# Kernel tuning notes

Hardware: AMD Instinct MI355X
Metric: run time of the kernel (lower is better)

The kernel has to match this reference:

```python
import jax, jax.numpy as jnp
import numpy as np

S, B, H = 2048, 16, 512      # seq_len, batch, hidden_size
L = 4096                     # total labels across batch
SMAX = 16                    # max span length
LAB = 256                    # label_size
V = 32000                    # len(voc)


def setup_inputs() -> dict:
    key = jax.random.key(0)
    ks = jax.random.split(key, 10)
    hidden = jax.random.normal(ks[0], (S, B, H), jnp.float32)
    begins = jax.random.randint(ks[1], (L,), 1, S - SMAX - 1)          # >=1 so begin-1 valid
    lens = jax.random.randint(ks[2], (L,), 1, SMAX + 1)                # span length in [1, SMAX]
    ends = begins + lens                                               # < S so hidden[end] valid
    bids = jax.random.randint(ks[3], (L,), 0, B)
    tags = jax.random.randint(ks[4], (L,), 0, V)
    sc = 0.02
    W1 = jax.random.normal(ks[5], (3 * H, LAB), jnp.float32) * sc
    b1 = jnp.zeros((LAB,), jnp.float32)
    W2 = jax.random.normal(ks[6], (LAB, LAB), jnp.float32) * sc
    b2 = jnp.zeros((LAB,), jnp.float32)
    Wo = jax.random.normal(ks[7], (LAB, V), jnp.float32) * sc
    bo = jnp.zeros((V,), jnp.float32)
    return dict(hidden=hidden, begins=begins, ends=ends, bids=bids, tags=tags,
                W1=W1, b1=b1, W2=W2, b2=b2, Wo=Wo, bo=bo)


def reference(hidden, begins, ends, bids, tags, W1, b1, W2, b2, Wo, bo):
    # --- batched span embed: gather + masked mean + boundary concat ---
    pos = begins[:, None] + jnp.arange(SMAX)            # [L, SMAX]
    valid = (pos < ends[:, None]).astype(hidden.dtype)  # [L, SMAX]
    posc = jnp.minimum(pos, S - 1)
    g = hidden[posc, bids[:, None]]                     # [L, SMAX, H] gather
    span_len = (ends - begins).astype(hidden.dtype)[:, None]
    mean = (g * valid[..., None]).sum(axis=1) / span_len           # [L, H]
    left = hidden[begins - 1, bids]                                 # [L, H]
    right = hidden[ends, bids]                                      # [L, H]
    span_emb = jnp.concatenate([left, mean, right], axis=-1)        # [L, 3H]
    # --- hidden2feature: Linear -> sigmoid -> Linear (dropout = eval identity) ---
    feat = jax.nn.sigmoid(span_emb @ W1 + b1) @ W2 + b2             # [L, LAB]
    # --- SoftmaxLoss: -log_softmax(h2o(feat)).gather(tags).mean() per label ---
    logp = jax.nn.log_softmax(feat @ Wo + bo, axis=-1)              # [L, V]
    per_label = -logp[jnp.arange(L), tags]                          # one tag per label
    return per_label.sum() / (L + 1e-5)
```

## Files before the change

### kernel.cpp

```cpp
#include <hip/hip_runtime.h>
#include <math.h>

#define S 2048
#define B 16
#define H 512
#define L 4096
#define SMAX 16
#define LAB 256
#define V 32000
#define NCH 250
#define LOG2E 1.44269504f

typedef __attribute__((ext_vector_type(8))) short short8;
typedef __attribute__((ext_vector_type(4))) float float4v;

__device__ inline ushort f2bf(float x) {
  union { float f; unsigned u; } c; c.f = x;
  unsigned r = c.u + 0x7fffu + ((c.u >> 16) & 1u);
  return (ushort)(r >> 16);
}
__device__ inline float bf2f(ushort h) {
  union { unsigned u; float f; } c; c.u = ((unsigned)h) << 16;
  return c.f;
}

__global__ __launch_bounds__(256) void spanb_kernel(
    const float* __restrict__ hidden, const int* __restrict__ begins,
    const int* __restrict__ ends, const int* __restrict__ bids,
    ushort* __restrict__ spanb) {
  int sub = threadIdx.x >> 7, t = threadIdx.x & 127;
  int l = blockIdx.x * 2 + sub;
  int b = bids[l], s0 = begins[l], s1 = ends[l];
  const float4* hidv = (const float4*)hidden;
  float4 lf = hidv[((size_t)(s0 - 1) * B + b) * 128 + t];
  float4 rf = hidv[((size_t)s1 * B + b) * 128 + t];
  float4 m = make_float4(0.f, 0.f, 0.f, 0.f);
  int len = s1 - s0;
  for (int j = 0; j < len; ++j) {
    float4 g = hidv[((size_t)(s0 + j) * B + b) * 128 + t];
    m.x += g.x; m.y += g.y; m.z += g.z; m.w += g.w;
  }
  float inv = 1.0f / (float)len;
  ushort* sp = spanb + (size_t)l * 1536;
  ushort4 u;
  u.x = f2bf(lf.x); u.y = f2bf(lf.y); u.z = f2bf(lf.z); u.w = f2bf(lf.w);
  *(ushort4*)&sp[t * 4] = u;
  u.x = f2bf(m.x * inv); u.y = f2bf(m.y * inv);
  u.z = f2bf(m.z * inv); u.w = f2bf(m.w * inv);
  *(ushort4*)&sp[512 + t * 4] = u;
  u.x = f2bf(rf.x); u.y = f2bf(rf.y); u.z = f2bf(rf.z); u.w = f2bf(rf.w);
  *(ushort4*)&sp[1024 + t * 4] = u;
}

__global__ __launch_bounds__(256) void tcast_kernel(
    const float* __restrict__ src, ushort* __restrict__ dst, int K, int N) {
  __shared__ ushort tile[64 * 72];
  int t = threadIdx.x;
  int n0 = blockIdx.x * 64;
  int k0 = blockIdx.y * 64;
  #pragma unroll
  for (int p = 0; p < 16; ++p) {
    int k = p * 4 + (t >> 6);
    int n = t & 63;
    tile[n * 72 + k] = f2bf(src[(size_t)(k0 + k) * N + n0 + n]);
  }
  __syncthreads();
  #pragma unroll
  for (int p = 0; p < 2; ++p) {
    int idx = p * 256 + t;
    int n = idx >> 3, c = idx & 7;
    *(uint4*)&dst[(size_t)(n0 + n) * K + k0 + c * 8] =
        *(const uint4*)&tile[n * 72 + c * 8];
  }
}

__global__ __launch_bounds__(256) void tcast_wo_kernel(
    const float* __restrict__ src, ushort* __restrict__ dst) {
  __shared__ ushort tile[64 * 72];
  int t = threadIdx.x;
  int n0 = blockIdx.x * 64;
  int k0 = blockIdx.y * 64;
  #pragma unroll
  for (int p = 0; p < 16; ++p) {
    int k = p * 4 + (t >> 6);
    int n = t & 63;
    tile[n * 72 + k] = f2bf(src[(size_t)(k0 + k) * V + n0 + n]);
  }
  __syncthreads();
  #pragma unroll
  for (int p = 0; p < 2; ++p) {
    int idx = p * 256 + t;
    int n = idx >> 3, c8 = idx & 7;
    int v = n0 + n, k = k0 + c8 * 8;
    int c = v >> 7, nt = (v >> 4) & 7, lr = v & 15;
    int kh = k >> 7, k4 = (k >> 5) & 3, lq = (k >> 3) & 3;
    size_t f = ((((size_t)c * 2 + kh) * 4 + k4) * 8 + nt) * 64 + lq * 16 + lr;
    *(uint4*)&dst[f * 8] = *(const uint4*)&tile[n * 72 + c8 * 8];
  }
}

__global__ __launch_bounds__(256) void feat_mfma_kernel(
    const ushort* __restrict__ spanb, const ushort* __restrict__ W1b,
    const float* __restrict__ b1, const ushort* __restrict__ W2b,
    const float* __restrict__ b2, ushort* __restrict__ featb) {
  __shared__ ushort Hs[16 * 264];
  int tid = threadIdx.x;
  int w = tid >> 6, lane = tid & 63;
  int lr = lane & 15, lq = lane >> 4;
  int l0 = blockIdx.x * 16;

  const short8* arow = (const short8*)(spanb + (size_t)(l0 + lr) * 1536 + lq * 8);
  const short8* brow[4];
  #pragma unroll
  for (int nt = 0; nt < 4; ++nt)
    brow[nt] = (const short8*)(W1b + (size_t)(w * 64 + nt * 16 + lr) * 1536 + lq * 8);

  float4v acc[4];
  float4v zero = {0.f, 0.f, 0.f, 0.f};
  #pragma unroll
  for (int nt = 0; nt < 4; ++nt) acc[nt] = zero;

  short8 af[2], bf[2][4];
  af[0] = arow[0];
  #pragma unroll
  for (int nt = 0; nt < 4; ++nt) bf[0][nt] = brow[nt][0];

  #pragma unroll
  for (int s = 0; s < 48; ++s) {
    int cur = s & 1, nxt = cur ^ 1;
    if (s < 47) {
      af[nxt] = arow[(s + 1) * 4];
      #pragma unroll
      for (int nt = 0; nt < 4; ++nt) bf[nxt][nt] = brow[nt][(s + 1) * 4];
    }
    #pragma unroll
    for (int nt = 0; nt < 4; ++nt)
      acc[nt] = __builtin_amdgcn_mfma_f32_16x16x32_bf16(
          af[cur], bf[cur][nt], acc[nt], 0, 0, 0);
  }

  {
    #pragma unroll
    for (int nt = 0; nt < 4; ++nt) {
      float b1v = b1[w * 64 + nt * 16 + lr];
      #pragma unroll
      for (int r = 0; r < 4; ++r) {
        int row = lq * 4 + r;
        float h = 1.0f / (1.0f + __expf(-(acc[nt][r] + b1v)));
        Hs[row * 264 + w * 64 + nt * 16 + lr] = f2bf(h);
      }
    }
  }
  __syncthreads();

  const short8* wrow[4];
  #pragma unroll
  for (int nt = 0; nt < 4; ++nt)
    wrow[nt] = (const short8*)(W2b + (size_t)(w * 64 + nt * 16 + lr) * 256 + lq * 8);

  float4v acc2[4];
  #pragma unroll
  for (int nt = 0; nt < 4; ++nt) acc2[nt] = zero;

  short8 bf2[2][4];
  #pragma unroll
  for (int nt = 0; nt < 4; ++nt) bf2[0][nt] = wrow[nt][0];

  #pragma unroll
  for (int s = 0; s < 8; ++s) {
    int cur = s & 1, nxt = cur ^ 1;
    if (s < 7) {
      #pragma unroll
      for (int nt = 0; nt < 4; ++nt) bf2[nxt][nt] = wrow[nt][(s + 1) * 4];
    }
    short8 af2 = *(const short8*)&Hs[lr * 264 + s * 32 + lq * 8];
    #pragma unroll
    for (int nt = 0; nt < 4; ++nt)
      acc2[nt] = __builtin_amdgcn_mfma_f32_16x16x32_bf16(
          af2, bf2[cur][nt], acc2[nt], 0, 0, 0);
  }

  {
    #pragma unroll
    for (int nt = 0; nt < 4; ++nt) {
      float b2v = b2[w * 64 + nt * 16 + lr];
      #pragma unroll
      for (int r = 0; r < 4; ++r) {
        int row = lq * 4 + r;
        int col = w * 64 + nt * 16 + lr;
        featb[(size_t)(l0 + row) * 256 + col] = f2bf(acc2[nt][r] + b2v);
      }
    }
  }
}

__global__ __launch_bounds__(256, 4) void logits2_kernel(
    const ushort* __restrict__ featb, const ushort* __restrict__ Wob,
    const float* __restrict__ bo, float* __restrict__ pz) {
  __shared__ ushort Blds[16384];
  int tid = threadIdx.x;
  int w = tid >> 6, lane = tid & 63;
  int lr = lane & 15, lq = lane >> 4;
  int l0 = blockIdx.x * 128;
  int v0 = blockIdx.y * 128;

  const short8* aptr[2];
  #pragma unroll
  for (int mt = 0; mt < 2; ++mt)
    aptr[mt] = (const short8*)(featb +
        (size_t)(l0 + w * 32 + mt * 16 + lr) * 256 + lq * 8);

  float4v acc[2][8];
  float4v zero = {0.f, 0.f, 0.f, 0.f};
  #pragma unroll
  for (int mt = 0; mt < 2; ++mt)
    #pragma unroll
    for (int nt = 0; nt < 8; ++nt) acc[mt][nt] = zero;

  short8 af[2][2];
  #pragma unroll
  for (int mt = 0; mt < 2; ++mt) af[0][mt] = aptr[mt][0];

  #pragma unroll
  for (int kh = 0; kh < 2; ++kh) {
    {
      const uint4* src4 = (const uint4*)(Wob +
          (size_t)blockIdx.y * 32768 + (size_t)kh * 16384);
      #pragma unroll
      for (int p = 0; p < 8; ++p) {
        int idx = p * 256 + tid;
        __builtin_amdgcn_global_load_lds(
            (const __attribute__((address_space(1))) unsigned int*)(src4 + idx),
            (__attribute__((address_space(3))) unsigned int*)&Blds[(size_t)idx * 8],
            16, 0, 0);
      }
    }
    __syncthreads();
    #pragma unroll
    for (int k4 = 0; k4 < 4; ++k4) {
      int kg = kh * 4 + k4;
      int cur = kg & 1, nxt = cur ^ 1;
      if (kg < 7) {
        #pragma unroll
        for (int mt = 0; mt < 2; ++mt)
          af[nxt][mt] = aptr[mt][(kg + 1) * 4];
      }
      short8 bf[8];
      #pragma unroll
      for (int nt = 0; nt < 8; ++nt)
        bf[nt] = *(const short8*)&Blds[(size_t)(((k4 * 8 + nt) * 64) + lane) * 8];
      __builtin_amdgcn_s_setprio(1);
      #pragma unroll
      for (int mt = 0; mt < 2; ++mt)
        #pragma unroll
        for (int nt = 0; nt < 8; ++nt)
          acc[mt][nt] = __builtin_amdgcn_mfma_f32_16x16x32_bf16(
              af[cur][mt], bf[nt], acc[mt][nt], 0, 0, 0);
      __builtin_amdgcn_s_setprio(0);
    }
    if (kh == 0) __syncthreads();
  }

  float bov[8];
  #pragma unroll
  for (int nt = 0; nt < 8; ++nt)
    bov[nt] = bo[v0 + nt * 16 + lr] * LOG2E;
  float z[2][4];
  #pragma unroll
  for (int mt = 0; mt < 2; ++mt)
    #pragma unroll
    for (int r = 0; r < 4; ++r) z[mt][r] = 0.f;
  #pragma unroll
  for (int mt = 0; mt < 2; ++mt)
    #pragma unroll
    for (int nt = 0; nt < 8; ++nt)
      #pragma unroll
      for (int r = 0; r < 4; ++r)
        z[mt][r] += exp2f(fmaf(acc[mt][nt][r], LOG2E, bov[nt]));
  #pragma unroll
  for (int mt = 0; mt < 2; ++mt)
    #pragma unroll
    for (int r = 0; r < 4; ++r) {
      #pragma unroll
      for (int off = 1; off < 16; off <<= 1)
        z[mt][r] += __shfl_xor(z[mt][r], off);
    }
  if (lr == 0) {
    int ch = blockIdx.y;
    #pragma unroll
    for (int mt = 0; mt < 2; ++mt) {
      float4 v4;
      v4.x = z[mt][0]; v4.y = z[mt][1]; v4.z = z[mt][2]; v4.w = z[mt][3];
      *(float4*)&pz[(size_t)ch * L + l0 + w * 32 + mt * 16 + lq * 4] = v4;
    }
  }
}

__global__ __launch_bounds__(256) void tag_kernel(
    const ushort* __restrict__ featb, const ushort* __restrict__ Wob,
    const float* __restrict__ bo, const int* __restrict__ tags,
    float* __restrict__ tagl) {
  int l = blockIdx.x * 4 + (threadIdx.x >> 6);
  int lane = threadIdx.x & 63;
  int tg = tags[l];
  int c = tg >> 7, nt = (tg >> 4) & 7, lr = tg & 15;
  int k0 = lane << 2;
  int kh = k0 >> 7, k4 = (k0 >> 5) & 3, lq = (k0 >> 3) & 3, e = k0 & 7;
  size_t f = ((((size_t)c * 2 + kh) * 4 + k4) * 8 + nt) * 64 + lq * 16 + lr;
  ushort4 wa = *(const ushort4*)&Wob[f * 8 + e];
  ushort4 fa = *(const ushort4*)&featb[(size_t)l * 256 + k0];
  float s = bf2f(fa.x) * bf2f(wa.x) + bf2f(fa.y) * bf2f(wa.y) +
            bf2f(fa.z) * bf2f(wa.z) + bf2f(fa.w) * bf2f(wa.w);
  #pragma unroll
  for (int off = 1; off < 64; off <<= 1) s += __shfl_xor(s, off);
  if (lane == 0) tagl[l] = s + bo[tg];
}

__global__ __launch_bounds__(256) void reduce_kernel(
    const float* __restrict__ pz, const float* __restrict__ tagl,
    float* __restrict__ out) {
  int l = blockIdx.x * 256 + threadIdx.x;
  float z = 0.f;
  for (int c = 0; c < NCH; ++c) z += pz[(size_t)c * L + l];
  float per = logf(z) - tagl[l];
  float v = per * (1.0f / (4096.0f + 1e-5f));
  #pragma unroll
  for (int off = 1; off < 64; off <<= 1) v += __shfl_xor(v, off);
  __shared__ float wsum[4];
  if ((threadIdx.x & 63) == 0) wsum[threadIdx.x >> 6] = v;
  __syncthreads();
  if (threadIdx.x == 0)
    atomicAdd(out, wsum[0] + wsum[1] + wsum[2] + wsum[3]);
}

extern "C" void kernel_launch(void* const* d_in, const int* in_sizes, int n_in,
                              void* d_out, int out_size, void* d_ws,
                              size_t ws_size, hipStream_t stream) {
  const float* hidden = (const float*)d_in[0];
  const int* begins = (const int*)d_in[1];
  const int* ends = (const int*)d_in[2];
  const int* bids = (const int*)d_in[3];
  const int* tags = (const int*)d_in[4];
  const float* W1 = (const float*)d_in[5];
  const float* b1 = (const float*)d_in[6];
  const float* W2 = (const float*)d_in[7];
  const float* b2 = (const float*)d_in[8];
  const float* Wo = (const float*)d_in[9];
  const float* bo = (const float*)d_in[10];
  float* out = (float*)d_out;

  ushort* featb = (ushort*)d_ws;
  ushort* Wob = featb + (size_t)L * 256;
  ushort* spanb = Wob + (size_t)V * 256;
  ushort* W1b = spanb + (size_t)L * 1536;
  ushort* W2b = W1b + (size_t)256 * 1536;
  float* pz = (float*)spanb;
  float* tagl = (float*)(W2b + (size_t)256 * 256);

  hipMemsetAsync(d_out, 0, sizeof(float), stream);
  spanb_kernel<<<L / 2, 256, 0, stream>>>(hidden, begins, ends, bids, spanb);
  tcast_kernel<<<dim3(4, 24), 256, 0, stream>>>(W1, W1b, 1536, LAB);
  tcast_kernel<<<dim3(4, 4), 256, 0, stream>>>(W2, W2b, LAB, LAB);
  tcast_wo_kernel<<<dim3(500, 4), 256, 0, stream>>>(Wo, Wob);
  feat_mfma_kernel<<<256, 256, 0, stream>>>(spanb, W1b, b1, W2b, b2, featb);
  logits2_kernel<<<dim3(32, NCH), 256, 0, stream>>>(featb, Wob, bo, pz);
  tag_kernel<<<L / 4, 256, 0, stream>>>(featb, Wob, bo, tags, tagl);
  reduce_kernel<<<L / 256, 256, 0, stream>>>(pz, tagl, out);
}
```

Before: 289.7 us.

## Merge prep kernels, fold tag dot into logits, process two vocab chunks per block

Span-embedding and the three weight cast/transposes are merged into one prep launch dispatched by block index. The memset is replaced by a write from the feature kernel, and the tag-logit kernel is folded into the logits launch as extra blocks. Each logits block now handles two 128-wide vocab chunks, prefetching the next chunk's first half while running the previous epilogue. This cuts launch count and hides some staging latency, at the cost of halving the logits grid and adding branch-divergent block roles.

```diff
diff --git a/kernel.cpp b/kernel.cpp
--- a/kernel.cpp
+++ b/kernel.cpp
@@ -24,40 +24,54 @@
   return c.f;
 }
 
-__global__ __launch_bounds__(256) void spanb_kernel(
+__global__ __launch_bounds__(256) void prep_kernel(
     const float* __restrict__ hidden, const int* __restrict__ begins,
     const int* __restrict__ ends, const int* __restrict__ bids,
-    ushort* __restrict__ spanb) {
-  int sub = threadIdx.x >> 7, t = threadIdx.x & 127;
-  int l = blockIdx.x * 2 + sub;
-  int b = bids[l], s0 = begins[l], s1 = ends[l];
-  const float4* hidv = (const float4*)hidden;
-  float4 lf = hidv[((size_t)(s0 - 1) * B + b) * 128 + t];
-  float4 rf = hidv[((size_t)s1 * B + b) * 128 + t];
-  float4 m = make_float4(0.f, 0.f, 0.f, 0.f);
-  int len = s1 - s0;
-  for (int j = 0; j < len; ++j) {
-    float4 g = hidv[((size_t)(s0 + j) * B + b) * 128 + t];
-    m.x += g.x; m.y += g.y; m.z += g.z; m.w += g.w;
-  }
-  float inv = 1.0f / (float)len;
-  ushort* sp = spanb + (size_t)l * 1536;
-  ushort4 u;
-  u.x = f2bf(lf.x); u.y = f2bf(lf.y); u.z = f2bf(lf.z); u.w = f2bf(lf.w);
-  *(ushort4*)&sp[t * 4] = u;
-  u.x = f2bf(m.x * inv); u.y = f2bf(m.y * inv);
-  u.z = f2bf(m.z * inv); u.w = f2bf(m.w * inv);
-  *(ushort4*)&sp[512 + t * 4] = u;
-  u.x = f2bf(rf.x); u.y = f2bf(rf.y); u.z = f2bf(rf.z); u.w = f2bf(rf.w);
-  *(ushort4*)&sp[1024 + t * 4] = u;
-}
-
-__global__ __launch_bounds__(256) void tcast_kernel(
-    const float* __restrict__ src, ushort* __restrict__ dst, int K, int N) {
+    ushort* __restrict__ spanb, const float* __restrict__ W1,
+    ushort* __restrict__ W1b, const float* __restrict__ W2,
+    ushort* __restrict__ W2b, const float* __restrict__ Wo,
+    ushort* __restrict__ Wob) {
   __shared__ ushort tile[64 * 72];
+  int bid = blockIdx.x;
   int t = threadIdx.x;
-  int n0 = blockIdx.x * 64;
-  int k0 = blockIdx.y * 64;
+
+  if (bid < 2048) {
+    int sub = t >> 7, tt = t & 127;
+    int l = bid * 2 + sub;
+    int b = bids[l], s0 = begins[l], s1 = ends[l];
+    const float4* hidv = (const float4*)hidden;
+    float4 lf = hidv[((size_t)(s0 - 1) * B + b) * 128 + tt];
+    float4 rf = hidv[((size_t)s1 * B + b) * 128 + tt];
+    float4 m = make_float4(0.f, 0.f, 0.f, 0.f);
+    int len = s1 - s0;
+    for (int j = 0; j < len; ++j) {
+      float4 g = hidv[((size_t)(s0 + j) * B + b) * 128 + tt];
+      m.x += g.x; m.y += g.y; m.z += g.z; m.w += g.w;
+    }
+    float inv = 1.0f / (float)len;
+    ushort* sp = spanb + (size_t)l * 1536;
+    ushort4 u;
+    u.x = f2bf(lf.x); u.y = f2bf(lf.y); u.z = f2bf(lf.z); u.w = f2bf(lf.w);
+    *(ushort4*)&sp[tt * 4] = u;
+    u.x = f2bf(m.x * inv); u.y = f2bf(m.y * inv);
+    u.z = f2bf(m.z * inv); u.w = f2bf(m.w * inv);
+    *(ushort4*)&sp[512 + tt * 4] = u;
+    u.x = f2bf(rf.x); u.y = f2bf(rf.y); u.z = f2bf(rf.z); u.w = f2bf(rf.w);
+    *(ushort4*)&sp[1024 + tt * 4] = u;
+    return;
+  }
+
+  const float* src; ushort* dst; int K, N, n0, k0; bool wo = false;
+  if (bid < 2144) {
+    int u = bid - 2048; src = W1; dst = W1b; K = 1536; N = 256;
+    n0 = (u & 3) * 64; k0 = (u >> 2) * 64;
+  } else if (bid < 2160) {
+    int u = bid - 2144; src = W2; dst = W2b; K = 256; N = 256;
+    n0 = (u & 3) * 64; k0 = (u >> 2) * 64;
+  } else {
+    int u = bid - 2160; src = Wo; dst = Wob; K = 256; N = V;
+    n0 = (u % 500) * 64; k0 = (u / 500) * 64; wo = true;
+  }
   #pragma unroll
   for (int p = 0; p < 16; ++p) {
     int k = p * 4 + (t >> 6);
@@ -65,46 +79,36 @@
     tile[n * 72 + k] = f2bf(src[(size_t)(k0 + k) * N + n0 + n]);
   }
   __syncthreads();
-  #pragma unroll
-  for (int p = 0; p < 2; ++p) {
-    int idx = p * 256 + t;
-    int n = idx >> 3, c = idx & 7;
-    *(uint4*)&dst[(size_t)(n0 + n) * K + k0 + c * 8] =
-        *(const uint4*)&tile[n * 72 + c * 8];
-  }
-}
-
-__global__ __launch_bounds__(256) void tcast_wo_kernel(
-    const float* __restrict__ src, ushort* __restrict__ dst) {
-  __shared__ ushort tile[64 * 72];
-  int t = threadIdx.x;
-  int n0 = blockIdx.x * 64;
-  int k0 = blockIdx.y * 64;
-  #pragma unroll
-  for (int p = 0; p < 16; ++p) {
-    int k = p * 4 + (t >> 6);
-    int n = t & 63;
-    tile[n * 72 + k] = f2bf(src[(size_t)(k0 + k) * V + n0 + n]);
-  }
-  __syncthreads();
-  #pragma unroll
-  for (int p = 0; p < 2; ++p) {
-    int idx = p * 256 + t;
-    int n = idx >> 3, c8 = idx & 7;
-    int v = n0 + n, k = k0 + c8 * 8;
-    int c = v >> 7, nt = (v >> 4) & 7, lr = v & 15;
-    int kh = k >> 7, k4 = (k >> 5) & 3, lq = (k >> 3) & 3;
-    size_t f = ((((size_t)c * 2 + kh) * 4 + k4) * 8 + nt) * 64 + lq * 16 + lr;
-    *(uint4*)&dst[f * 8] = *(const uint4*)&tile[n * 72 + c8 * 8];
+  if (!wo) {
+    #pragma unroll
+    for (int p = 0; p < 2; ++p) {
+      int idx = p * 256 + t;
+      int n = idx >> 3, c = idx & 7;
+      *(uint4*)&dst[(size_t)(n0 + n) * K + k0 + c * 8] =
+          *(const uint4*)&tile[n * 72 + c * 8];
+    }
+  } else {
+    #pragma unroll
+    for (int p = 0; p < 2; ++p) {
+      int idx = p * 256 + t;
+      int n = idx >> 3, c8 = idx & 7;
+      int v = n0 + n, k = k0 + c8 * 8;
+      int c = v >> 7, nt = (v >> 4) & 7, lr = v & 15;
+      int kh = k >> 7, k4 = (k >> 5) & 3, lq = (k >> 3) & 3;
+      size_t f = ((((size_t)c * 2 + kh) * 4 + k4) * 8 + nt) * 64 + lq * 16 + lr;
+      *(uint4*)&dst[f * 8] = *(const uint4*)&tile[n * 72 + c8 * 8];
+    }
   }
 }
 
 __global__ __launch_bounds__(256) void feat_mfma_kernel(
     const ushort* __restrict__ spanb, const ushort* __restrict__ W1b,
     const float* __restrict__ b1, const ushort* __restrict__ W2b,
-    const float* __restrict__ b2, ushort* __restrict__ featb) {
+    const float* __restrict__ b2, ushort* __restrict__ featb,
+    float* __restrict__ out) {
   __shared__ ushort Hs[16 * 264];
   int tid = threadIdx.x;
+  if (blockIdx.x == 0 && tid == 0) *out = 0.f;
   int w = tid >> 6, lane = tid & 63;
   int lr = lane & 15, lq = lane >> 4;
   int l0 = blockIdx.x * 16;
@@ -194,15 +198,38 @@
   }
 }
 
-__global__ __launch_bounds__(256, 4) void logits2_kernel(
+__global__ __launch_bounds__(256, 4) void logits_kernel(
     const ushort* __restrict__ featb, const ushort* __restrict__ Wob,
-    const float* __restrict__ bo, float* __restrict__ pz) {
+    const float* __restrict__ bo, const int* __restrict__ tags,
+    float* __restrict__ pz, float* __restrict__ tagl) {
   __shared__ ushort Blds[16384];
+  int bid = blockIdx.x;
   int tid = threadIdx.x;
-  int w = tid >> 6, lane = tid & 63;
+  int lane = tid & 63;
   int lr = lane & 15, lq = lane >> 4;
-  int l0 = blockIdx.x * 128;
-  int v0 = blockIdx.y * 128;
+
+  if (bid >= 4000) {
+    int l = (bid - 4000) * 4 + (tid >> 6);
+    int tg = tags[l];
+    int c = tg >> 7, nt = (tg >> 4) & 7, tlr = tg & 15;
+    int k0 = lane << 2;
+    int kh = k0 >> 7, k4 = (k0 >> 5) & 3, tlq = (k0 >> 3) & 3, e = k0 & 7;
+    size_t f = ((((size_t)c * 2 + kh) * 4 + k4) * 8 + nt) * 64 + tlq * 16 + tlr;
+    ushort4 wa = *(const ushort4*)&Wob[f * 8 + e];
+    ushort4 fa = *(const ushort4*)&featb[(size_t)l * 256 + k0];
+    float s = bf2f(fa.x) * bf2f(wa.x) + bf2f(fa.y) * bf2f(wa.y) +
+              bf2f(fa.z) * bf2f(wa.z) + bf2f(fa.w) * bf2f(wa.w);
+    #pragma unroll
+    for (int off = 1; off < 64; off <<= 1) s += __shfl_xor(s, off);
+    if (lane == 0) tagl[l] = s + bo[tg];
+    return;
+  }
+
+  int w = tid >> 6;
+  int lb = bid & 31;
+  int cpair = bid >> 5;
+  int c0 = cpair * 2, c1 = c0 + 1;
+  int l0 = lb * 128;
 
   const short8* aptr[2];
   #pragma unroll
@@ -221,99 +248,112 @@
   #pragma unroll
   for (int mt = 0; mt < 2; ++mt) af[0][mt] = aptr[mt][0];
 
-  #pragma unroll
-  for (int kh = 0; kh < 2; ++kh) {
-    {
-      const uint4* src4 = (const uint4*)(Wob +
-          (size_t)blockIdx.y * 32768 + (size_t)kh * 16384);
-      #pragma unroll
-      for (int p = 0; p < 8; ++p) {
-        int idx = p * 256 + tid;
-        __builtin_amdgcn_global_load_lds(
-            (const __attribute__((address_space(1))) unsigned int*)(src4 + idx),
-            (__attribute__((address_space(3))) unsigned int*)&Blds[(size_t)idx * 8],
-            16, 0, 0);
-      }
-    }
-    __syncthreads();
-    #pragma unroll
-    for (int k4 = 0; k4 < 4; ++k4) {
-      int kg = kh * 4 + k4;
-      int cur = kg & 1, nxt = cur ^ 1;
-      if (kg < 7) {
-        #pragma unroll
-        for (int mt = 0; mt < 2; ++mt)
-          af[nxt][mt] = aptr[mt][(kg + 1) * 4];
-      }
-      short8 bf[8];
-      #pragma unroll
-      for (int nt = 0; nt < 8; ++nt)
-        bf[nt] = *(const short8*)&Blds[(size_t)(((k4 * 8 + nt) * 64) + lane) * 8];
-      __builtin_amdgcn_s_setprio(1);
-      #pragma unroll
-      for (int mt = 0; mt < 2; ++mt)
-        #pragma unroll
-        for (int nt = 0; nt < 8; ++nt)
-          acc[mt][nt] = __builtin_amdgcn_mfma_f32_16x16x32_bf16(
-              af[cur][mt], bf[nt], acc[mt][nt], 0, 0, 0);
-      __builtin_amdgcn_s_setprio(0);
-    }
-    if (kh == 0) __syncthreads();
-  }
+#define STAGE_HALF(ch, kh)                                                    \
+  {                                                                           \
+    const uint4* src4 = (const uint4*)(Wob +                                  \
+        (size_t)(ch) * 32768 + (size_t)(kh) * 16384);                         \
+    _Pragma("unroll")                                                         \
+    for (int p = 0; p < 8; ++p) {                                             \
+      int idx = p * 256 + tid;                                                \
+      __builtin_amdgcn_global_load_lds(                                       \
+          (const __attribute__((address_space(1))) unsigned int*)(src4 + idx),\
+          (__attribute__((address_space(3))) unsigned int*)&Blds[(size_t)idx * 8], \
+          16, 0, 0);                                                          \
+    }                                                                         \
+  }
+
+#define KG_BLOCK(kh)                                                          \
+  _Pragma("unroll")                                                           \
+  for (int k4 = 0; k4 < 4; ++k4) {                                            \
+    int kg = (kh) * 4 + k4;                                                   \
+    int cur = kg & 1, nxt = cur ^ 1;                                          \
+    if (kg < 7) {                                                             \
+      _Pragma("unroll")                                                       \
+      for (int mt = 0; mt < 2; ++mt)                                          \
+        af[nxt][mt] = aptr[mt][(kg + 1) * 4];                                 \
+    }                                                                         \
+    short8 bf[8];                                                             \
+    _Pragma("unroll")                                                         \
+    for (int nt = 0; nt < 8; ++nt)                                            \
+      bf[nt] = *(const short8*)&Blds[(size_t)(((k4 * 8 + nt) * 64) + lane) * 8]; \
+    __builtin_amdgcn_s_setprio(1);                                            \
+    _Pragma("unroll")                                                         \
+    for (int mt = 0; mt < 2; ++mt)                                            \
+      _Pragma("unroll")                                                       \
+      for (int nt = 0; nt < 8; ++nt)                                          \
+        acc[mt][nt] = __builtin_amdgcn_mfma_f32_16x16x32_bf16(                \
+            af[cur][mt], bf[nt], acc[mt][nt], 0, 0, 0);                       \
+    __builtin_amdgcn_s_setprio(0);                                            \
+  }
+
+#define EPILOGUE(ch)                                                          \
+  {                                                                           \
+    float z[2][4];                                                            \
+    _Pragma("unroll")                                                         \
+    for (int mt = 0; mt < 2; ++mt)                                            \
+      _Pragma("unroll")                                                       \
+      for (int r = 0; r < 4; ++r) z[mt][r] = 0.f;                             \
+    _Pragma("unroll")                                                         \
+    for (int mt = 0; mt < 2; ++mt)                                            \
+      _Pragma("unroll")                                                       \
+      for (int nt = 0; nt < 8; ++nt)                                          \
+        _Pragma("unroll")                                                     \
+        for (int r = 0; r < 4; ++r)                                           \
+          z[mt][r] += exp2f(fmaf(acc[mt][nt][r], LOG2E, bov[nt]));            \
+    _Pragma("unroll")                                                         \
+    for (int mt = 0; mt < 2; ++mt)                                            \
+      _Pragma("unroll")                                                       \
+      for (int r = 0; r < 4; ++r) {                                           \
+        _Pragma("unroll")                                                     \
+        for (int off = 1; off < 16; off <<= 1)                                \
+          z[mt][r] += __shfl_xor(z[mt][r], off);                              \
+      }                                                                       \
+    if (lr == 0) {                                                            \
+      _Pragma("unroll")                                                       \
+      for (int mt = 0; mt < 2; ++mt) {                                        \
+        float4 v4;                                                            \
+        v4.x = z[mt][0]; v4.y = z[mt][1]; v4.z = z[mt][2]; v4.w = z[mt][3];   \
+        *(float4*)&pz[(size_t)(ch) * L + l0 + w * 32 + mt * 16 + lq * 4] = v4;\
+      }                                                                       \
+    }                                                                         \
+  }
+
+  STAGE_HALF(c0, 0);
+  __syncthreads();
+  KG_BLOCK(0);
+  __syncthreads();
+  STAGE_HALF(c0, 1);
+  __syncthreads();
+  KG_BLOCK(1);
 
   float bov[8];
   #pragma unroll
   for (int nt = 0; nt < 8; ++nt)
-    bov[nt] = bo[v0 + nt * 16 + lr] * LOG2E;
-  float z[2][4];
+    bov[nt] = bo[c0 * 128 + nt * 16 + lr] * LOG2E;
+  #pragma unroll
+  for (int mt = 0; mt < 2; ++mt) af[0][mt] = aptr[mt][0];
+  __syncthreads();
+  STAGE_HALF(c1, 0);
+  EPILOGUE(c0);
   #pragma unroll
   for (int mt = 0; mt < 2; ++mt)
     #pragma unroll
-    for (int r = 0; r < 4; ++r) z[mt][r] = 0.f;
-  #pragma unroll
-  for (int mt = 0; mt < 2; ++mt)
-    #pragma unroll
-    for (int nt = 0; nt < 8; ++nt)
-      #pragma unroll
-      for (int r = 0; r < 4; ++r)
-        z[mt][r] += exp2f(fmaf(acc[mt][nt][r], LOG2E, bov[nt]));
-  #pragma unroll
-  for (int mt = 0; mt < 2; ++mt)
-    #pragma unroll
-    for (int r = 0; r < 4; ++r) {
-      #pragma unroll
-      for (int off = 1; off < 16; off <<= 1)
-        z[mt][r] += __shfl_xor(z[mt][r], off);
-    }
-  if (lr == 0) {
-    int ch = blockIdx.y;
-    #pragma unroll
-    for (int mt = 0; mt < 2; ++mt) {
-      float4 v4;
-      v4.x = z[mt][0]; v4.y = z[mt][1]; v4.z = z[mt][2]; v4.w = z[mt][3];
-      *(float4*)&pz[(size_t)ch * L + l0 + w * 32 + mt * 16 + lq * 4] = v4;
-    }
-  }
-}
-
-__global__ __launch_bounds__(256) void tag_kernel(
-    const ushort* __restrict__ featb, const ushort* __restrict__ Wob,
-    const float* __restrict__ bo, const int* __restrict__ tags,
-    float* __restrict__ tagl) {
-  int l = blockIdx.x * 4 + (threadIdx.x >> 6);
-  int lane = threadIdx.x & 63;
-  int tg = tags[l];
-  int c = tg >> 7, nt = (tg >> 4) & 7, lr = tg & 15;
-  int k0 = lane << 2;
-  int kh = k0 >> 7, k4 = (k0 >> 5) & 3, lq = (k0 >> 3) & 3, e = k0 & 7;
-  size_t f = ((((size_t)c * 2 + kh) * 4 + k4) * 8 + nt) * 64 + lq * 16 + lr;
-  ushort4 wa = *(const ushort4*)&Wob[f * 8 + e];
-  ushort4 fa = *(const ushort4*)&featb[(size_t)l * 256 + k0];
-  float s = bf2f(fa.x) * bf2f(wa.x) + bf2f(fa.y) * bf2f(wa.y) +
-            bf2f(fa.z) * bf2f(wa.z) + bf2f(fa.w) * bf2f(wa.w);
-  #pragma unroll
-  for (int off = 1; off < 64; off <<= 1) s += __shfl_xor(s, off);
-  if (lane == 0) tagl[l] = s + bo[tg];
+    for (int nt = 0; nt < 8; ++nt) acc[mt][nt] = zero;
+  __syncthreads();
+
+  KG_BLOCK(0);
+  __syncthreads();
+  STAGE_HALF(c1, 1);
+  __syncthreads();
+  KG_BLOCK(1);
+  #pragma unroll
+  for (int nt = 0; nt < 8; ++nt)
+    bov[nt] = bo[c1 * 128 + nt * 16 + lr] * LOG2E;
+  EPILOGUE(c1);
+
+#undef STAGE_HALF
+#undef KG_BLOCK
+#undef EPILOGUE
 }
 
 __global__ __launch_bounds__(256) void reduce_kernel(
@@ -357,13 +397,10 @@
   float* pz = (float*)spanb;
   float* tagl = (float*)(W2b + (size_t)256 * 256);
 
-  hipMemsetAsync(d_out, 0, sizeof(float), stream);
-  spanb_kernel<<<L / 2, 256, 0, stream>>>(hidden, begins, ends, bids, spanb);
-  tcast_kernel<<<dim3(4, 24), 256, 0, stream>>>(W1, W1b, 1536, LAB);
-  tcast_kernel<<<dim3(4, 4), 256, 0, stream>>>(W2, W2b, LAB, LAB);
-  tcast_wo_kernel<<<dim3(500, 4), 256, 0, stream>>>(Wo, Wob);
-  feat_mfma_kernel<<<256, 256, 0, stream>>>(spanb, W1b, b1, W2b, b2, featb);
-  logits2_kernel<<<dim3(32, NCH), 256, 0, stream>>>(featb, Wob, bo, pz);
-  tag_kernel<<<L / 4, 256, 0, stream>>>(featb, Wob, bo, tags, tagl);
+  prep_kernel<<<4160, 256, 0, stream>>>(hidden, begins, ends, bids, spanb,
+                                        W1, W1b, W2, W2b, Wo, Wob);
+  feat_mfma_kernel<<<256, 256, 0, stream>>>(spanb, W1b, b1, W2b, b2, featb,
+                                            out);
+  logits_kernel<<<5024, 256, 0, stream>>>(featb, Wob, bo, tags, pz, tagl);
   reduce_kernel<<<L / 256, 256, 0, stream>>>(pz, tagl, out);
 }
```

After: 287.5 us. About the same (-0.8%).
